# Performance work log

Measured on AMD Instinct MI355X. Metric: run time of the kernel, lower is better.

The kernel has to match this reference:

```python
import jax, jax.numpy as jnp
import numpy as np
import math

N, V, NH = 4096, 256, 64  # samples, variables (channels), hidden units


def _permutation_skeleton(v):
    # perm[c] is a (V, V-1) selection matrix keeping all variables j != c,
    # columns ordered by j (faithful to CustomizedRelaModule.permutation_matrix
    # with skeleton = 1 - I, so max_dim = V - 1 and no zero-padding remains).
    perm = np.zeros((v, v, v - 1), dtype=np.float32)
    for c in range(v):
        idx = np.delete(np.arange(v), c)
        perm[c, idx, np.arange(v - 1)] = 1.0
    return jnp.asarray(perm)


def setup_inputs() -> dict:
    key = jax.random.key(0)
    k = jax.random.split(key, 7)
    data = jax.random.normal(k[0], (N, V), dtype=jnp.float32)
    adj = jax.random.normal(k[1], (V, V), dtype=jnp.float32)        # self.adj_matrix ~ N(0,1)
    neurons = jax.random.normal(k[2], (NH, V), dtype=jnp.float32)   # self.neurons ~ N(0,1)
    s1 = 1.0 / math.sqrt(V - 1)  # input_layer: uniform(-1/sqrt(in), 1/sqrt(in)), in = max_dim = V-1
    w_in = jax.random.uniform(k[3], (V, V - 1, NH), minval=-s1, maxval=s1, dtype=jnp.float32)
    b_in = jax.random.uniform(k[4], (V, NH), minval=-s1, maxval=s1, dtype=jnp.float32)
    s2 = 1.0 / math.sqrt(NH)
    w_out = jax.random.uniform(k[5], (V, NH, 1), minval=-s2, maxval=s2, dtype=jnp.float32)
    b_out = jax.random.uniform(k[6], (V, 1), minval=-s2, maxval=s2, dtype=jnp.float32)
    perm = _permutation_skeleton(V)
    return {"data": data, "adj": adj, "neurons": neurons,
            "w_in": w_in, "b_in": b_in, "w_out": w_out, "b_out": b_out,
            "perm": perm}


def reference(data, adj, neurons, w_in, b_in, w_out, b_out, perm):
    # categorical_matrix is identity, so the adjacency passed is adj itself.
    # Linear3D input layer with adj + permutation:
    #   masked[n, c, k] = sum_j data[n, j] * adj[j, c] * perm[c, j, k]
    # i.e. per channel c, gather adj-weighted inputs for all j != c.
    masked = jnp.einsum('nj,jc,cjk->nck', data, adj, perm)  # (N, V, V-1)
    # per-channel linear + tanh
    h = jnp.tanh(jnp.einsum('nck,ckh->nch', masked, w_in) + b_in[None])  # (N, V, NH)
    # output Linear3D with adj_matrix = neurons (NH, V): elementwise gate then per-channel linear
    gated = h * neurons.T[None]  # (N, V, NH)
    out = jnp.einsum('nch,cho->nco', gated, w_out) + b_out[None]  # (N, V, 1)
    return (adj, out[..., 0])
```

## Files before the change

### kernel.cpp

```cpp
#include <hip/hip_runtime.h>
#include <hip/hip_bf16.h>

#define NS   4096
#define NV   256
#define NHID 64
#define K2F  2.8853900817779268f

typedef short s8v __attribute__((ext_vector_type(8)));
typedef float f4v __attribute__((ext_vector_type(4)));

typedef __attribute__((address_space(1))) const unsigned int GU;
typedef __attribute__((address_space(3))) unsigned int LU;

__device__ __forceinline__ void gload16(const void* gp, void* lp) {
    __builtin_amdgcn_global_load_lds((GU*)gp, (LU*)lp, 16, 0, 0);
}

__device__ __forceinline__ unsigned short f2bf(float x) {
    __hip_bfloat16 h = __float2bfloat16(x);
    return *reinterpret_cast<unsigned short*>(&h);
}

__global__ __launch_bounds__(256) void k_prep_all(
        const float* __restrict__ adj, const float* __restrict__ w_in,
        unsigned short* __restrict__ W2t,
        const float* __restrict__ data, unsigned short* __restrict__ dataB,
        float* __restrict__ out0,
        const float* __restrict__ neurons, const float* __restrict__ w_out,
        const float* __restrict__ b_out, float* __restrict__ g2, float* __restrict__ BO,
        const float* __restrict__ b_in, float* __restrict__ bi2)
{
    __shared__ float t[64][65];
    const int blk = blockIdx.x, tid = threadIdx.x;
    if (blk < 1024) {
        int c  = blk >> 2;
        int k0 = (blk & 3) * 64;
#pragma unroll
        for (int i = 0; i < 16; ++i) {
            int lin = i * 256 + tid;
            int kr = lin >> 6, h = lin & 63;
            int k = k0 + kr;
            float v = 0.0f;
            if (k != c) {
                int m = k - (k > c ? 1 : 0);
                v = adj[k * NV + c] * w_in[((size_t)c * 255 + m) * 64 + h];
            }
            t[kr][h] = v;
        }
        __syncthreads();
#pragma unroll
        for (int i = 0; i < 16; ++i) {
            int lin = i * 256 + tid;
            int h = lin >> 6, kr = lin & 63;
            W2t[((size_t)(c * 64 + h)) * NV + k0 + kr] = f2bf(t[kr][h]);
        }
        return;
    }
    const int b = blk - 1024;
    if (b < 1024) {
        int i = b * 256 + tid;
        float4 v = reinterpret_cast<const float4*>(data)[i];
        ushort4 o = make_ushort4(f2bf(v.x), f2bf(v.y), f2bf(v.z), f2bf(v.w));
        reinterpret_cast<ushort4*>(dataB)[i] = o;
    } else if (b < 1088) {
        int i = (b - 1024) * 256 + tid;
        reinterpret_cast<float4*>(out0)[i] = reinterpret_cast<const float4*>(adj)[i];
    } else if (b < 1152) {
        int j = (b - 1088) * 256 + tid;
        int c = j >> 6, h = j & 63;
        float gv = neurons[h * NV + c] * w_out[j];
        g2[j] = 2.0f * gv;
        float s = gv;
        s += __shfl_xor(s, 1);  s += __shfl_xor(s, 2);  s += __shfl_xor(s, 4);
        s += __shfl_xor(s, 8);  s += __shfl_xor(s, 16); s += __shfl_xor(s, 32);
        if ((tid & 63) == 0) BO[c] = b_out[c] + s;
    } else {
        int i = (b - 1152) * 256 + tid;
        float4 v = reinterpret_cast<const float4*>(b_in)[i];
        v.x *= K2F; v.y *= K2F; v.z *= K2F; v.w *= K2F;
        reinterpret_cast<float4*>(bi2)[i] = v;
    }
}

__global__ __launch_bounds__(256, 2) void k_gemm_fused(
        const unsigned short* __restrict__ dataB,
        const unsigned short* __restrict__ W2t,
        const float* __restrict__ g2,
        const float* __restrict__ bi2,
        const float* __restrict__ BO,
        float* __restrict__ out1)
{
    __shared__ __align__(16) char lds[49152];
    const int tid  = threadIdx.x;
    const int w    = tid >> 6;
    const int lane = tid & 63;
    const int lq   = lane >> 4, lr = lane & 15;

    const int orig = (int)blockIdx.x;
    const int swz  = (orig & 7) * 256 + (orig >> 3);
    const int bm0  = (swz & 31) << 7;
    const int bn0  = (swz >> 5) << 8;

    f4v acc[8][4];
#pragma unroll
    for (int mi = 0; mi < 8; ++mi)
#pragma unroll
        for (int ni = 0; ni < 4; ++ni)
            acc[mi][ni] = (f4v){0.f, 0.f, 0.f, 0.f};

    unsigned int offA[4], ldsoA[4], offB[8], ldsoB[8];
#pragma unroll
    for (int t = 0; t < 4; ++t) {
        int o = w * 4096 + t * 1024 + lane * 16;
        int row = o >> 7;
        int inner = (o & 127) ^ ((row & 7) << 4);
        ldsoA[t] = (unsigned)(w * 4096 + t * 1024);
        offA[t]  = (unsigned)(bm0 + row) * 512u + (unsigned)inner;
    }
#pragma unroll
    for (int t = 0; t < 8; ++t) {
        int o = w * 8192 + t * 1024 + lane * 16;
        int row = o >> 7;
        int inner = (o & 127) ^ ((row & 7) << 4);
        ldsoB[t] = (unsigned)(16384 + w * 8192 + t * 1024);
        offB[t]  = (unsigned)(bn0 + row) * 512u + (unsigned)inner;
    }

    const char* dA = (const char*)dataB;
    const char* dB = (const char*)W2t;

    for (int kt = 0; kt < 4; ++kt) {
#pragma unroll
        for (int t = 0; t < 4; ++t)
            gload16(dA + (size_t)offA[t] + kt * 128, lds + ldsoA[t]);
#pragma unroll
        for (int t = 0; t < 8; ++t)
            gload16(dB + (size_t)offB[t] + kt * 128, lds + ldsoB[t]);
        __syncthreads();

#pragma unroll
        for (int kk = 0; kk < 2; ++kk) {
            s8v afr[8], bfr[4];
#pragma unroll
            for (int mi = 0; mi < 8; ++mi) {
                int ml = mi * 16 + lr;
                int inner = (kk * 64 + (lq << 4)) ^ ((ml & 7) << 4);
                afr[mi] = *reinterpret_cast<const s8v*>(lds + ml * 128 + inner);
            }
#pragma unroll
            for (int ni = 0; ni < 4; ++ni) {
                int nl = w * 64 + ni * 16 + lr;
                int inner = (kk * 64 + (lq << 4)) ^ ((nl & 7) << 4);
                bfr[ni] = *reinterpret_cast<const s8v*>(lds + 16384 + nl * 128 + inner);
            }
            __builtin_amdgcn_s_setprio(1);
#pragma unroll
            for (int mi = 0; mi < 8; ++mi)
#pragma unroll
                for (int ni = 0; ni < 4; ++ni)
                    acc[mi][ni] = __builtin_amdgcn_mfma_f32_16x16x32_bf16(
                        bfr[ni], afr[mi], acc[mi][ni], 0, 0, 0);
            __builtin_amdgcn_s_setprio(0);
        }
        __syncthreads();
    }

    const int cidx = (bn0 >> 6) + w;
    float4 g2v[4], bi2v[4];
#pragma unroll
    for (int ni = 0; ni < 4; ++ni) {
        int base = cidx * 64 + ni * 16 + lq * 4;
        g2v[ni]  = *(const float4*)&g2 [base];
        bi2v[ni] = *(const float4*)&bi2[base];
    }
    const float BOv = BO[cidx];

    float s0, s1, s2, s3, s4, s5, s6, s7;
#define EPI_TERM(T, GC, BC, RR)                                                \
    { float mm = __builtin_fmaf(acc[mi][ni][RR], K2F, (BC));                   \
      float e  = __builtin_amdgcn_exp2f(mm);                                   \
      (T) = __builtin_fmaf((GC), __builtin_amdgcn_rcpf(e + 1.0f), (T)); }
#define EPI_MI(T, MI)                                                          \
    { const int mi = (MI); float t = 0.f;                                      \
      _Pragma("unroll")                                                        \
      for (int ni = 0; ni < 4; ++ni) {                                         \
          EPI_TERM(t, g2v[ni].x, bi2v[ni].x, 0);                               \
          EPI_TERM(t, g2v[ni].y, bi2v[ni].y, 1);                               \
          EPI_TERM(t, g2v[ni].z, bi2v[ni].z, 2);                               \
          EPI_TERM(t, g2v[ni].w, bi2v[ni].w, 3);                               \
      }                                                                        \
      t += __shfl_xor(t, 16);                                                  \
      t += __shfl_xor(t, 32);                                                  \
      (T) = t; }
    EPI_MI(s0, 0); EPI_MI(s1, 1); EPI_MI(s2, 2); EPI_MI(s3, 3);
    EPI_MI(s4, 4); EPI_MI(s5, 5); EPI_MI(s6, 6); EPI_MI(s7, 7);
#undef EPI_MI
#undef EPI_TERM
    float vlo = lane < 16 ? s0 : (lane < 32 ? s1 : (lane < 48 ? s2 : s3));
    float vhi = lane < 16 ? s4 : (lane < 32 ? s5 : (lane < 48 ? s6 : s7));
    out1[(unsigned)(bm0 + lane) * NV + cidx]      = BOv - vlo;
    out1[(unsigned)(bm0 + 64 + lane) * NV + cidx] = BOv - vhi;
}

extern "C" void kernel_launch(void* const* d_in, const int* in_sizes, int n_in,
                              void* d_out, int out_size, void* d_ws, size_t ws_size,
                              hipStream_t stream) {
    const float* data    = (const float*)d_in[0];
    const float* adj     = (const float*)d_in[1];
    const float* neurons = (const float*)d_in[2];
    const float* w_in    = (const float*)d_in[3];
    const float* b_in    = (const float*)d_in[4];
    const float* w_out   = (const float*)d_in[5];
    const float* b_out   = (const float*)d_in[6];

    float* out0 = (float*)d_out;
    float* out1 = out0 + NV * NV;

    unsigned short* dataB = (unsigned short*)d_ws;
    unsigned short* W2t   = (unsigned short*)((char*)d_ws + 2097152);
    float*          g2    = (float*)((char*)d_ws + 10485760);
    float*          bi2   = (float*)((char*)d_ws + 10551296);
    float*          BO    = (float*)((char*)d_ws + 10616832);

    hipLaunchKernelGGL(k_prep_all, dim3(2192), dim3(256), 0, stream,
                       adj, w_in, W2t, data, dataB, out0,
                       neurons, w_out, b_out, g2, BO, b_in, bi2);
    hipLaunchKernelGGL(k_gemm_fused, dim3(2048), dim3(256), 0, stream,
                       dataB, W2t, g2, bi2, BO, out1);
}
```

Before: 55.87 us.

## Warp-specialize GEMM with producer waves and triple-buffered LDS pipeline

Each block grows to 512 threads. Four producer waves issue async global-to-LDS loads into three 48KB buffers and signal with raw barriers, while four consumer waves only run MFMA. The consumer tile is remapped to a 2x2 wave grid (64x128 per wave) and the epilogue covers two channels per wave. The aim is to overlap load latency with compute. In exchange it needs 144KB of dynamic LDS per block, which likely allows only one block per CU and halves the compute waves per CU.

```diff
diff --git a/kernel.cpp b/kernel.cpp
--- a/kernel.cpp
+++ b/kernel.cpp
@@ -82,7 +82,7 @@
     }
 }
 
-__global__ __launch_bounds__(256, 2) void k_gemm_fused(
+__global__ __launch_bounds__(512, 2) void k_gemm_fused(
         const unsigned short* __restrict__ dataB,
         const unsigned short* __restrict__ W2t,
         const float* __restrict__ g2,
@@ -90,7 +90,7 @@
         const float* __restrict__ BO,
         float* __restrict__ out1)
 {
-    __shared__ __align__(16) char lds[49152];
+    extern __shared__ __align__(16) char lds[];
     const int tid  = threadIdx.x;
     const int w    = tid >> 6;
     const int lane = tid & 63;
@@ -101,83 +101,102 @@
     const int bm0  = (swz & 31) << 7;
     const int bn0  = (swz >> 5) << 8;
 
-    f4v acc[8][4];
-#pragma unroll
-    for (int mi = 0; mi < 8; ++mi)
-#pragma unroll
-        for (int ni = 0; ni < 4; ++ni)
+    if (w >= 4) {
+        const int ptid = tid - 256;
+        const int pw   = ptid >> 6;
+        unsigned offA[4], ldsoA[4], offB[8], ldsoB[8];
+#pragma unroll
+        for (int t = 0; t < 4; ++t) {
+            int o = pw * 4096 + t * 1024 + lane * 16;
+            int row = o >> 7;
+            int inner = (o & 127) ^ ((row & 7) << 4);
+            ldsoA[t] = (unsigned)(pw * 4096 + t * 1024);
+            offA[t]  = (unsigned)(bm0 + row) * 512u + (unsigned)inner;
+        }
+#pragma unroll
+        for (int t = 0; t < 8; ++t) {
+            int o = pw * 8192 + t * 1024 + lane * 16;
+            int row = o >> 7;
+            int inner = (o & 127) ^ ((row & 7) << 4);
+            ldsoB[t] = (unsigned)(16384 + pw * 8192 + t * 1024);
+            offB[t]  = (unsigned)(bn0 + row) * 512u + (unsigned)inner;
+        }
+        const char* dA = (const char*)dataB;
+        const char* dB = (const char*)W2t;
+
+#define STAGE(KT, BUFO)                                                        \
+        do {                                                                   \
+            _Pragma("unroll")                                                  \
+            for (int t = 0; t < 4; ++t)                                        \
+                gload16(dA + (size_t)offA[t] + (KT) * 128, lds + (BUFO) + ldsoA[t]); \
+            _Pragma("unroll")                                                  \
+            for (int t = 0; t < 8; ++t)                                        \
+                gload16(dB + (size_t)offB[t] + (KT) * 128, lds + (BUFO) + ldsoB[t]); \
+        } while (0)
+
+        STAGE(0, 0);
+        STAGE(1, 49152);
+        asm volatile("s_waitcnt vmcnt(12)" ::: "memory");
+        __builtin_amdgcn_s_barrier();
+        STAGE(2, 98304);
+        asm volatile("s_waitcnt vmcnt(0)" ::: "memory");
+        __builtin_amdgcn_s_barrier();
+        STAGE(3, 0);
+        asm volatile("s_waitcnt vmcnt(0)" ::: "memory");
+        __builtin_amdgcn_s_barrier();
+#undef STAGE
+        return;
+    }
+
+    const int wr = w >> 1, wc = w & 1;
+
+    f4v acc[4][8];
+#pragma unroll
+    for (int mi = 0; mi < 4; ++mi)
+#pragma unroll
+        for (int ni = 0; ni < 8; ++ni)
             acc[mi][ni] = (f4v){0.f, 0.f, 0.f, 0.f};
 
-    unsigned int offA[4], ldsoA[4], offB[8], ldsoB[8];
-#pragma unroll
-    for (int t = 0; t < 4; ++t) {
-        int o = w * 4096 + t * 1024 + lane * 16;
-        int row = o >> 7;
-        int inner = (o & 127) ^ ((row & 7) << 4);
-        ldsoA[t] = (unsigned)(w * 4096 + t * 1024);
-        offA[t]  = (unsigned)(bm0 + row) * 512u + (unsigned)inner;
-    }
-#pragma unroll
-    for (int t = 0; t < 8; ++t) {
-        int o = w * 8192 + t * 1024 + lane * 16;
-        int row = o >> 7;
-        int inner = (o & 127) ^ ((row & 7) << 4);
-        ldsoB[t] = (unsigned)(16384 + w * 8192 + t * 1024);
-        offB[t]  = (unsigned)(bn0 + row) * 512u + (unsigned)inner;
-    }
-
-    const char* dA = (const char*)dataB;
-    const char* dB = (const char*)W2t;
-
-    for (int kt = 0; kt < 4; ++kt) {
-#pragma unroll
-        for (int t = 0; t < 4; ++t)
-            gload16(dA + (size_t)offA[t] + kt * 128, lds + ldsoA[t]);
-#pragma unroll
-        for (int t = 0; t < 8; ++t)
-            gload16(dB + (size_t)offB[t] + kt * 128, lds + ldsoB[t]);
-        __syncthreads();
-
-#pragma unroll
-        for (int kk = 0; kk < 2; ++kk) {
-            s8v afr[8], bfr[4];
-#pragma unroll
-            for (int mi = 0; mi < 8; ++mi) {
-                int ml = mi * 16 + lr;
-                int inner = (kk * 64 + (lq << 4)) ^ ((ml & 7) << 4);
-                afr[mi] = *reinterpret_cast<const s8v*>(lds + ml * 128 + inner);
-            }
-#pragma unroll
-            for (int ni = 0; ni < 4; ++ni) {
-                int nl = w * 64 + ni * 16 + lr;
-                int inner = (kk * 64 + (lq << 4)) ^ ((nl & 7) << 4);
-                bfr[ni] = *reinterpret_cast<const s8v*>(lds + 16384 + nl * 128 + inner);
-            }
-            __builtin_amdgcn_s_setprio(1);
-#pragma unroll
-            for (int mi = 0; mi < 8; ++mi)
-#pragma unroll
-                for (int ni = 0; ni < 4; ++ni)
-                    acc[mi][ni] = __builtin_amdgcn_mfma_f32_16x16x32_bf16(
-                        bfr[ni], afr[mi], acc[mi][ni], 0, 0, 0);
-            __builtin_amdgcn_s_setprio(0);
-        }
-        __syncthreads();
-    }
-
-    const int cidx = (bn0 >> 6) + w;
-    float4 g2v[4], bi2v[4];
-#pragma unroll
-    for (int ni = 0; ni < 4; ++ni) {
-        int base = cidx * 64 + ni * 16 + lq * 4;
-        g2v[ni]  = *(const float4*)&g2 [base];
-        bi2v[ni] = *(const float4*)&bi2[base];
-    }
-    const float BOv = BO[cidx];
-
-    float s0, s1, s2, s3, s4, s5, s6, s7;
+#define COMPUTE(BUFO)                                                          \
+    do {                                                                       \
+        _Pragma("unroll")                                                      \
+        for (int kk = 0; kk < 2; ++kk) {                                       \
+            s8v afr[4], bfr[8];                                                \
+            _Pragma("unroll")                                                  \
+            for (int mi = 0; mi < 4; ++mi) {                                   \
+                int ml = wr * 64 + mi * 16 + lr;                               \
+                int inner = (kk * 64 + (lq << 4)) ^ ((ml & 7) << 4);           \
+                afr[mi] = *reinterpret_cast<const s8v*>(lds + (BUFO) + ml * 128 + inner); \
+            }                                                                  \
+            _Pragma("unroll")                                                  \
+            for (int ni = 0; ni < 8; ++ni) {                                   \
+                int nl = wc * 128 + ni * 16 + lr;                              \
+                int inner = (kk * 64 + (lq << 4)) ^ ((nl & 7) << 4);           \
+                bfr[ni] = *reinterpret_cast<const s8v*>(lds + (BUFO) + 16384 + nl * 128 + inner); \
+            }                                                                  \
+            __builtin_amdgcn_s_setprio(1);                                     \
+            _Pragma("unroll")                                                  \
+            for (int mi = 0; mi < 4; ++mi) {                                   \
+                _Pragma("unroll")                                              \
+                for (int ni = 0; ni < 8; ++ni)                                 \
+                    acc[mi][ni] = __builtin_amdgcn_mfma_f32_16x16x32_bf16(     \
+                        bfr[ni], afr[mi], acc[mi][ni], 0, 0, 0);               \
+            }                                                                  \
+            __builtin_amdgcn_s_setprio(0);                                     \
+        }                                                                      \
+    } while (0)
+
+    __builtin_amdgcn_s_barrier();
+    COMPUTE(0);
+    __builtin_amdgcn_s_barrier();
+    COMPUTE(49152);
+    __builtin_amdgcn_s_barrier();
+    COMPUTE(98304);
+    COMPUTE(0);
+#undef COMPUTE
+
 #define EPI_TERM(T, GC, BC, RR)                                                \
-    { float mm = __builtin_fmaf(acc[mi][ni][RR], K2F, (BC));                   \
+    { float mm = __builtin_fmaf(acc[mi][nb + ni][RR], K2F, (BC));              \
       float e  = __builtin_amdgcn_exp2f(mm);                                   \
       (T) = __builtin_fmaf((GC), __builtin_amdgcn_rcpf(e + 1.0f), (T)); }
 #define EPI_MI(T, MI)                                                          \
@@ -192,14 +211,26 @@
       t += __shfl_xor(t, 16);                                                  \
       t += __shfl_xor(t, 32);                                                  \
       (T) = t; }
-    EPI_MI(s0, 0); EPI_MI(s1, 1); EPI_MI(s2, 2); EPI_MI(s3, 3);
-    EPI_MI(s4, 4); EPI_MI(s5, 5); EPI_MI(s6, 6); EPI_MI(s7, 7);
+
+#pragma unroll
+    for (int ch = 0; ch < 2; ++ch) {
+        const int nb   = ch * 4;
+        const int cidx = (bn0 >> 6) + wc * 2 + ch;
+        float4 g2v[4], bi2v[4];
+#pragma unroll
+        for (int ni = 0; ni < 4; ++ni) {
+            int base = cidx * 64 + ni * 16 + lq * 4;
+            g2v[ni]  = *(const float4*)&g2 [base];
+            bi2v[ni] = *(const float4*)&bi2[base];
+        }
+        const float BOv = BO[cidx];
+        float s0, s1, s2, s3;
+        EPI_MI(s0, 0); EPI_MI(s1, 1); EPI_MI(s2, 2); EPI_MI(s3, 3);
+        float v = lane < 16 ? s0 : (lane < 32 ? s1 : (lane < 48 ? s2 : s3));
+        out1[(unsigned)(bm0 + wr * 64 + lane) * NV + cidx] = BOv - v;
+    }
 #undef EPI_MI
 #undef EPI_TERM
-    float vlo = lane < 16 ? s0 : (lane < 32 ? s1 : (lane < 48 ? s2 : s3));
-    float vhi = lane < 16 ? s4 : (lane < 32 ? s5 : (lane < 48 ? s6 : s7));
-    out1[(unsigned)(bm0 + lane) * NV + cidx]      = BOv - vlo;
-    out1[(unsigned)(bm0 + 64 + lane) * NV + cidx] = BOv - vhi;
 }
 
 extern "C" void kernel_launch(void* const* d_in, const int* in_sizes, int n_in,
@@ -225,6 +256,6 @@
     hipLaunchKernelGGL(k_prep_all, dim3(2192), dim3(256), 0, stream,
                        adj, w_in, W2t, data, dataB, out0,
                        neurons, w_out, b_out, g2, BO, b_in, bi2);
-    hipLaunchKernelGGL(k_gemm_fused, dim3(2048), dim3(256), 0, stream,
+    hipLaunchKernelGGL(k_gemm_fused, dim3(2048), dim3(512), 147456, stream,
                        dataB, W2t, g2, bi2, BO, out1);
 }
```

New measurement: 66.16 us. 18.4% more time.
